# Kernel optimization log

Hardware: AMD Instinct MI355X
Metric: run time of the kernel (lower is better)

The kernel has to match this reference:

```python
import jax, jax.numpy as jnp
import numpy as np

N_NODES = 16384
N_EDGES = 65536
N_GRAPHS = 512
F_XD = 78
HEADS = 10
HID = F_XD * HEADS  # 780
SEQ = 1000
EMB = 100
VOCAB = 8000
NF = 32
KS = 8
CLEN = EMB - KS + 1  # 93
OUT_DIM = 128


def setup_inputs():
    key = jax.random.key(0)
    keys = jax.random.split(key, 32)
    it = iter(keys)

    def rn(shape, scale=0.05):
        return jax.random.normal(next(it), shape, dtype=jnp.float32) * scale

    x = jax.random.normal(next(it), (N_NODES, F_XD), dtype=jnp.float32)
    edge_index = jax.random.randint(next(it), (2, N_EDGES), 0, N_NODES)
    batch = jnp.sort(jax.random.randint(next(it), (N_NODES,), 0, N_GRAPHS))
    target = jax.random.randint(next(it), (N_GRAPHS, SEQ), 0, VOCAB)
    return {
        "x": x, "edge_index": edge_index, "batch": batch, "target": target,
        "gat_w": rn((F_XD, HID)), "gat_att_src": rn((HEADS, F_XD)),
        "gat_att_dst": rn((HEADS, F_XD)), "gat_b": rn((HID,)),
        "gcn_w": rn((HID, HID)), "gcn_b": rn((HID,)),
        "fcg1_w": rn((2 * HID, 1500)), "fcg1_b": rn((1500,)),
        "fcg2_w": rn((1500, OUT_DIM)), "fcg2_b": rn((OUT_DIM,)),
        "emb_w": rn((VOCAB, EMB), 1.0),
        "conv_w": rn((NF, SEQ, KS)), "conv_b": rn((NF,)),
        "fcxt_w": rn((NF * CLEN, OUT_DIM)), "fcxt_b": rn((OUT_DIM,)),
        "mlp1_w": rn((2 * OUT_DIM, 1024)), "mlp1_b": rn((1024,)),
        "mlp2_w": rn((1024, 512)), "mlp2_b": rn((512,)),
        "mlp3_w": rn((512, 1)), "mlp3_b": rn((1,)),
    }


def _forward(edge_index, batch, target, x, gat_w, gat_att_src, gat_att_dst, gat_b,
             gcn_w, gcn_b, fcg1_w, fcg1_b, fcg2_w, fcg2_b, emb_w, conv_w, conv_b,
             fcxt_w, fcxt_b, mlp1_w, mlp1_b, mlp2_w, mlp2_b, mlp3_w, mlp3_b):
    loops = jnp.arange(N_NODES)
    src = jnp.concatenate([edge_index[0], loops])  # add self-loops (PyG default)
    dst = jnp.concatenate([edge_index[1], loops])
    # --- GATConv(78 -> 78, heads=10, concat) ---
    xh = (x @ gat_w).reshape(N_NODES, HEADS, F_XD)
    a_src = jnp.einsum('nhc,hc->nh', xh, gat_att_src)
    a_dst = jnp.einsum('nhc,hc->nh', xh, gat_att_dst)
    e = jax.nn.leaky_relu(a_src[src] + a_dst[dst], 0.2)  # [E+N, H]
    emax = jax.ops.segment_max(e, dst, num_segments=N_NODES)
    ee = jnp.exp(e - emax[dst])
    den = jax.ops.segment_sum(ee, dst, num_segments=N_NODES)
    coef = ee / den[dst]  # segment softmax over incoming edges
    h = jax.ops.segment_sum(xh[src] * coef[:, :, None], dst, num_segments=N_NODES)
    h = jax.nn.relu(h.reshape(N_NODES, HID) + gat_b)
    # --- GCNConv(780 -> 780), symmetric normalization with self-loops ---
    hw = h @ gcn_w
    deg = jax.ops.segment_sum(jnp.ones((src.shape[0],), hw.dtype), dst, num_segments=N_NODES)
    dinv = jax.lax.rsqrt(jnp.maximum(deg, 1.0))  # deg >= 1 due to self-loops
    g = jax.ops.segment_sum(hw[src] * (dinv[src] * dinv[dst])[:, None], dst,
                            num_segments=N_NODES) + gcn_b
    g = jax.nn.relu(g)
    # --- global max / mean pool per graph ---
    gmp = jax.ops.segment_max(g, batch, num_segments=N_GRAPHS)
    cnt = jax.ops.segment_sum(jnp.ones((N_NODES,), g.dtype), batch, num_segments=N_GRAPHS)
    gap = jax.ops.segment_sum(g, batch, num_segments=N_GRAPHS) / jnp.maximum(cnt, 1.0)[:, None]
    d = jnp.concatenate([gmp, gap], axis=1)  # [B, 1560]
    d = jax.nn.relu(d @ fcg1_w + fcg1_b)     # dropout = eval-mode no-op
    d = d @ fcg2_w + fcg2_b                  # [B, 128]
    # --- protein branch: embedding + Conv1d(in=1000, out=32, k=8) + fc ---
    emb = emb_w[target]  # [B, SEQ=1000, EMB=100]
    c = jax.lax.conv_general_dilated(emb, conv_w, (1,), 'VALID',
                                     dimension_numbers=('NCH', 'OIH', 'NCH'))
    c = c + conv_b[None, :, None]            # [B, 32, 93]
    p = c.reshape(N_GRAPHS, NF * CLEN) @ fcxt_w + fcxt_b  # [B, 128]
    # --- fused MLP head: 256 -> 1024 -> 512 -> 1 ---
    o = jnp.concatenate([d, p], axis=1)
    o = jax.nn.relu(o @ mlp1_w + mlp1_b)
    o = jax.nn.relu(o @ mlp2_w + mlp2_b)
    return o @ mlp3_w + mlp3_b               # [B, 1]


def reference(x, edge_index, batch, target, gat_w, gat_att_src, gat_att_dst, gat_b,
              gcn_w, gcn_b, fcg1_w, fcg1_b, fcg2_w, fcg2_b, emb_w, conv_w, conv_b,
              fcxt_w, fcxt_b, mlp1_w, mlp1_b, mlp2_w, mlp2_b, mlp3_w, mlp3_b):
    return _forward(edge_index, batch, target, x, gat_w, gat_att_src, gat_att_dst,
                    gat_b, gcn_w, gcn_b, fcg1_w, fcg1_b, fcg2_w, fcg2_b, emb_w,
                    conv_w, conv_b, fcxt_w, fcxt_b, mlp1_w, mlp1_b, mlp2_w, mlp2_b,
                    mlp3_w, mlp3_b)
```

## Files before the change

### kernel.cpp

```cpp
#include <hip/hip_runtime.h>

#define NN 16384
#define NE 65536
#define NT 81920
#define NG 512
#define NH 10
#define FX 78
#define HD 780
#define SEQ 1000
#define EMB 100
#define NF 32
#define KS 8
#define CLEN 93

typedef __bf16 bf16x8 __attribute__((ext_vector_type(8)));
typedef float  f32x4  __attribute__((ext_vector_type(4)));

__global__ __launch_bounds__(256)
void cast_pad_a(const float* __restrict__ in, __bf16* __restrict__ out,
                int M, int K, int Kp)
{
    size_t idx = (size_t)blockIdx.x*256 + threadIdx.x;
    if (idx >= (size_t)M*Kp) return;
    int r = idx / Kp, c = idx % Kp;
    out[idx] = (c < K) ? (__bf16)in[(size_t)r*K + c] : (__bf16)0.f;
}

__global__ __launch_bounds__(256)
void cast_pad_bt(const float* __restrict__ B, __bf16* __restrict__ out,
                 int K, int N, int Kp, int Np)
{
    size_t idx = (size_t)blockIdx.x*256 + threadIdx.x;
    if (idx >= (size_t)Np*Kp) return;
    int n = idx / Kp, k = idx % Kp;
    out[idx] = (n < N && k < K) ? (__bf16)B[(size_t)k*N + n] : (__bf16)0.f;
}

#define BKP 40
template<bool BIAS, bool RELU, bool BF16OUT>
__global__ __launch_bounds__(256)
void gemm_mfma(const __bf16* __restrict__ A, const __bf16* __restrict__ Bt,
               const float* __restrict__ bias, void* __restrict__ Cv,
               int M, int N, int Kp, int ldc, int Nz)
{
    __shared__ __align__(16) __bf16 As[128*BKP];
    __shared__ __align__(16) __bf16 Bs[128*BKP];
    const int tid = threadIdx.x;
    const int row0 = blockIdx.y*128, col0 = blockIdx.x*128;
    const int lane = tid & 63, wid = tid >> 6;
    const int wm = wid & 1, wn = wid >> 1;
    const int l15 = lane & 15, lk = lane >> 4;

    f32x4 acc[4][4];
#pragma unroll
    for (int i = 0; i < 4; i++)
#pragma unroll
        for (int j = 0; j < 4; j++) acc[i][j] = (f32x4){0.f,0.f,0.f,0.f};

    for (int k0 = 0; k0 < Kp; k0 += 32) {
        __syncthreads();
#pragma unroll
        for (int it = 0; it < 2; ++it) {
            int c = tid + it*256;
            int r = c >> 2, c16 = c & 3;
            uint4 va = *(const uint4*)(A  + (size_t)(row0+r)*Kp + k0 + c16*8);
            *(uint4*)&As[r*BKP + c16*8] = va;
            uint4 vb = *(const uint4*)(Bt + (size_t)(col0+r)*Kp + k0 + c16*8);
            *(uint4*)&Bs[r*BKP + c16*8] = vb;
        }
        __syncthreads();
        bf16x8 af[4], bfr[4];
#pragma unroll
        for (int i = 0; i < 4; i++) {
            af[i]  = *(const bf16x8*)&As[(wm*64 + i*16 + l15)*BKP + lk*8];
            bfr[i] = *(const bf16x8*)&Bs[(wn*64 + i*16 + l15)*BKP + lk*8];
        }
#pragma unroll
        for (int i = 0; i < 4; i++)
#pragma unroll
            for (int j = 0; j < 4; j++)
                acc[i][j] = __builtin_amdgcn_mfma_f32_16x16x32_bf16(af[i], bfr[j], acc[i][j], 0, 0, 0);
    }

#pragma unroll
    for (int i = 0; i < 4; i++) {
        int rbase = row0 + wm*64 + i*16 + lk*4;
#pragma unroll
        for (int j = 0; j < 4; j++) {
            int cc = col0 + wn*64 + j*16 + l15;
            if (cc >= Nz) continue;
            bool real = cc < N;
            float bv = (BIAS && real) ? bias[cc] : 0.f;
#pragma unroll
            for (int r = 0; r < 4; r++) {
                float v = real ? (acc[i][j][r] + bv) : 0.f;
                if (RELU) v = v > 0.f ? v : 0.f;
                if (BF16OUT) ((__bf16*)Cv)[(size_t)(rbase + r)*ldc + cc] = (__bf16)v;
                else         ((float*) Cv)[(size_t)(rbase + r)*ldc + cc] = v;
            }
        }
    }
}

__global__ __launch_bounds__(256)
void gemm_mfma_splitk(const __bf16* __restrict__ A, const __bf16* __restrict__ Bt,
                      float* __restrict__ part, int M, int Kp, int ldp, int ksteps)
{
    __shared__ __align__(16) __bf16 As[128*BKP];
    __shared__ __align__(16) __bf16 Bs[128*BKP];
    const int tid = threadIdx.x;
    const int row0 = blockIdx.y*128, col0 = blockIdx.x*128;
    const int s = blockIdx.z;
    const int lane = tid & 63, wid = tid >> 6;
    const int wm = wid & 1, wn = wid >> 1;
    const int l15 = lane & 15, lk = lane >> 4;

    const int T = Kp >> 5;
    int kb = s*ksteps, ke = kb + ksteps;
    if (ke > T) ke = T;

    f32x4 acc[4][4];
#pragma unroll
    for (int i = 0; i < 4; i++)
#pragma unroll
        for (int j = 0; j < 4; j++) acc[i][j] = (f32x4){0.f,0.f,0.f,0.f};

    for (int kk = kb; kk < ke; kk++) {
        int k0 = kk*32;
        __syncthreads();
#pragma unroll
        for (int it = 0; it < 2; ++it) {
            int c = tid + it*256;
            int r = c >> 2, c16 = c & 3;
            uint4 va = *(const uint4*)(A  + (size_t)(row0+r)*Kp + k0 + c16*8);
            *(uint4*)&As[r*BKP + c16*8] = va;
            uint4 vb = *(const uint4*)(Bt + (size_t)(col0+r)*Kp + k0 + c16*8);
            *(uint4*)&Bs[r*BKP + c16*8] = vb;
        }
        __syncthreads();
        bf16x8 af[4], bfr[4];
#pragma unroll
        for (int i = 0; i < 4; i++) {
            af[i]  = *(const bf16x8*)&As[(wm*64 + i*16 + l15)*BKP + lk*8];
            bfr[i] = *(const bf16x8*)&Bs[(wn*64 + i*16 + l15)*BKP + lk*8];
        }
#pragma unroll
        for (int i = 0; i < 4; i++)
#pragma unroll
            for (int j = 0; j < 4; j++)
                acc[i][j] = __builtin_amdgcn_mfma_f32_16x16x32_bf16(af[i], bfr[j], acc[i][j], 0, 0, 0);
    }

#pragma unroll
    for (int i = 0; i < 4; i++) {
        int rbase = row0 + wm*64 + i*16 + lk*4;
#pragma unroll
        for (int j = 0; j < 4; j++) {
            int cc = col0 + wn*64 + j*16 + l15;
#pragma unroll
            for (int r = 0; r < 4; r++)
                part[((size_t)s*M + rbase + r)*ldp + cc] = acc[i][j][r];
        }
    }
}

template<bool RELU>
__global__ __launch_bounds__(256)
void reduce_splitk(const float* __restrict__ part, const float* __restrict__ bias,
                   __bf16* __restrict__ C, int M, int N, int ldp, int S,
                   int ldc, int Nz)
{
    int idx = blockIdx.x*256 + threadIdx.x;
    int nc4 = Nz >> 2;
    if (idx >= M*nc4) return;
    int r = idx / nc4, c = (idx - r*nc4)*4;
    float4 a = {0.f,0.f,0.f,0.f};
    for (int s = 0; s < S; s++) {
        float4 v = *(const float4*)(part + ((size_t)s*M + r)*ldp + c);
        a.x += v.x; a.y += v.y; a.z += v.z; a.w += v.w;
    }
    float vv[4] = {a.x, a.y, a.z, a.w};
    __bf16 o4[4];
#pragma unroll
    for (int j = 0; j < 4; j++) {
        float v = 0.f;
        if (c + j < N) {
            v = vv[j] + bias[c+j];
            if (RELU) v = v > 0.f ? v : 0.f;
        }
        o4[j] = (__bf16)v;
    }
    *(uint2*)&C[(size_t)r*ldc + c] = *(uint2*)o4;
}

__global__ __launch_bounds__(256)
void attn_logits(const __bf16* __restrict__ xh, const float* __restrict__ att_s,
                 const float* __restrict__ att_d,
                 float* __restrict__ a_src, float* __restrict__ a_dst)
{
    int idx = blockIdx.x*256 + threadIdx.x;
    if (idx >= NN*NH) return;
    int n = idx / NH, h = idx % NH;
    const __bf16* xr = xh + (size_t)n*800 + h*FX;
    const float* as = att_s + h*FX;
    const float* ad = att_d + h*FX;
    float s1 = 0.f, s2 = 0.f;
    for (int c = 0; c < FX; c++) {
        float v = (float)xr[c];
        s1 = fmaf(v, as[c], s1);
        s2 = fmaf(v, ad[c], s2);
    }
    a_src[idx] = s1;
    a_dst[idx] = s2;
}

__global__ void edge_count(const int* __restrict__ ei, int* __restrict__ deg)
{
    int e = blockIdx.x*256 + threadIdx.x;
    if (e >= NT) return;
    int dst = (e < NE) ? ei[NE + e] : (e - NE);
    atomicAdd(&deg[dst], 1);
}

__global__ __launch_bounds__(1024)
void scan_kernel(const int* __restrict__ deg, int* __restrict__ offs, int* __restrict__ cursor)
{
    __shared__ int part[1024];
    int tid = threadIdx.x;
    int base = tid*16;
    int v[16]; int ssum = 0;
#pragma unroll
    for (int j = 0; j < 16; j++) { v[j] = deg[base+j]; ssum += v[j]; }
    part[tid] = ssum;
    __syncthreads();
    for (int d = 1; d < 1024; d <<= 1) {
        int t = (tid >= d) ? part[tid-d] : 0;
        __syncthreads();
        part[tid] += t;
        __syncthreads();
    }
    int run = (tid == 0) ? 0 : part[tid-1];
#pragma unroll
    for (int j = 0; j < 16; j++) { offs[base+j] = run; cursor[base+j] = run; run += v[j]; }
    if (tid == 1023) offs[NN] = run;
}

__global__ void edge_scatter(const int* __restrict__ ei, int* __restrict__ cursor,
                             int* __restrict__ csr)
{
    int e = blockIdx.x*256 + threadIdx.x;
    if (e >= NT) return;
    int src, dst;
    if (e < NE) { src = ei[e]; dst = ei[NE + e]; }
    else        { src = e - NE; dst = e - NE; }
    int pos = atomicAdd(&cursor[dst], 1);
    csr[pos] = src;
}

__global__ void dinv_kernel(const int* __restrict__ offs, float* __restrict__ dinv)
{
    int n = blockIdx.x*256 + threadIdx.x;
    if (n >= NN) return;
    int d = offs[n+1] - offs[n];
    dinv[n] = rsqrtf((float)(d > 0 ? d : 1));
}

__global__ __launch_bounds__(256)
void gat_agg(const __bf16* __restrict__ xh, const float* __restrict__ a_src,
             const float* __restrict__ a_dst, const float* __restrict__ gat_b,
             const int* __restrict__ offs, const int* __restrict__ csr,
             __bf16* __restrict__ hbf)
{
    int n = blockIdx.x*4 + (threadIdx.x >> 6);
    if (n >= NN) return;
    int lane = threadIdx.x & 63;
    bool act = lane < 60;
    int h   = act ? (lane / 6) : 0;
    int sub = act ? (lane % 6) : 0;
    int cbase = h*FX + sub*13;
    int off = offs[n], end = offs[n+1];
    float adn = a_dst[n*NH + h];

    float m = -3.0e38f;
    for (int i = off; i < end; i++) {
        int s = csr[i];
        float ev = a_src[s*NH + h] + adn;
        ev = ev > 0.f ? ev : 0.2f*ev;
        m = fmaxf(m, ev);
    }
    float den = 0.f;
    float acc[13];
#pragma unroll
    for (int j = 0; j < 13; j++) acc[j] = 0.f;
    for (int i = off; i < end; i++) {
        int s = csr[i];
        float ev = a_src[s*NH + h] + adn;
        ev = ev > 0.f ? ev : 0.2f*ev;
        float ee = __expf(ev - m);
        den += ee;
        const __bf16* xr = xh + (size_t)s*800 + cbase;
#pragma unroll
        for (int j = 0; j < 13; j++) acc[j] = fmaf((float)xr[j], ee, acc[j]);
    }
    if (act) {
        float inv = 1.f / den;
        const float* bb = gat_b + cbase;
        __bf16* op = hbf + (size_t)n*800 + cbase;
#pragma unroll
        for (int j = 0; j < 13; j++) {
            float v = fmaf(acc[j], inv, bb[j]);
            op[j] = (__bf16)(v > 0.f ? v : 0.f);
        }
    } else {
        __bf16* op = hbf + (size_t)n*800 + 780 + (lane - 60)*5;
#pragma unroll
        for (int j = 0; j < 5; j++) op[j] = (__bf16)0.f;
    }
}

__global__ __launch_bounds__(256)
void gcn_agg(const __bf16* __restrict__ hw, const float* __restrict__ dinv,
             const float* __restrict__ gcn_b, const int* __restrict__ offs,
             const int* __restrict__ csr, __bf16* __restrict__ g)
{
    int n = blockIdx.x*4 + (threadIdx.x >> 6);
    if (n >= NN) return;
    int lane = threadIdx.x & 63;
    int off = offs[n], end = offs[n+1];
    float dn = dinv[n];
    float acc[13];
#pragma unroll
    for (int j = 0; j < 13; j++) acc[j] = 0.f;
    for (int i = off; i < end; i++) {
        int s = csr[i];
        float w = dinv[s] * dn;
        const __bf16* r = hw + (size_t)s*800;
#pragma unroll
        for (int j = 0; j < 13; j++) {
            int c = lane + 64*j;
            if (c < HD) acc[j] = fmaf((float)r[c], w, acc[j]);
        }
    }
    __bf16* op = g + (size_t)n*HD;
#pragma unroll
    for (int j = 0; j < 13; j++) {
        int c = lane + 64*j;
        if (c < HD) {
            float v = acc[j] + gcn_b[c];
            op[c] = (__bf16)(v > 0.f ? v : 0.f);
        }
    }
}

__global__ void gstart_kernel(const int* __restrict__ batch, int* __restrict__ goffs)
{
    int b = blockIdx.x*256 + threadIdx.x;
    if (b > NG) return;
    if (b == NG) { goffs[NG] = NN; return; }
    int lo = 0, hi = NN;
    while (lo < hi) { int mid = (lo+hi) >> 1; if (batch[mid] < b) lo = mid+1; else hi = mid; }
    goffs[b] = lo;
}

__global__ __launch_bounds__(256)
void pool_kernel(const __bf16* __restrict__ g, const int* __restrict__ goffs,
                 __bf16* __restrict__ d)
{
    int b = blockIdx.x;
    int tid = threadIdx.x;
    int s = goffs[b], e = goffs[b+1];
    float mx[4], sm[4];
#pragma unroll
    for (int j = 0; j < 4; j++) { mx[j] = -3.0e38f; sm[j] = 0.f; }
    for (int n = s; n < e; n++) {
        const __bf16* r = g + (size_t)n*HD;
#pragma unroll
        for (int j = 0; j < 4; j++) {
            int c = tid + 256*j;
            if (c < HD) { float v = (float)r[c]; mx[j] = fmaxf(mx[j], v); sm[j] += v; }
        }
    }
    int cnt = e - s;
    float inv = 1.f / (float)(cnt > 0 ? cnt : 1);
#pragma unroll
    for (int j = 0; j < 4; j++) {
        int c = tid + 256*j;
        if (c < HD) {
            d[(size_t)b*1568 + c]      = (__bf16)mx[j];
            d[(size_t)b*1568 + HD + c] = (__bf16)(sm[j] * inv);
        }
    }
    if (tid < 8) d[(size_t)b*1568 + 1560 + tid] = (__bf16)0.f;
}

__global__ __launch_bounds__(256)
void emb_cast(const float* __restrict__ emb_w, __bf16* __restrict__ embbf)
{
    int idx = blockIdx.x*256 + threadIdx.x;
    if (idx >= 8001*112) return;
    int r = idx / 112, c = idx - (idx/112)*112;
    float v = (r < 8000 && c < EMB) ? emb_w[(size_t)r*EMB + c] : 0.f;
    embbf[idx] = (__bf16)v;
}

__global__ __launch_bounds__(256)
void conv_w_repack(const float* __restrict__ conv_w, __bf16* __restrict__ w2)
{
    int idx = blockIdx.x*256 + threadIdx.x;
    if (idx >= 256*1024) return;
    int op = idx >> 10, i = idx & 1023;
    int o = op & 31, k = op >> 5;
    w2[idx] = (i < SEQ) ? (__bf16)conv_w[((size_t)o*SEQ + i)*KS + k] : (__bf16)0.f;
}

#define CP 104
#define SB (112*40)

__global__ __launch_bounds__(512)
void conv_gemm2(const int* __restrict__ target, const __bf16* __restrict__ embbf,
                const __bf16* __restrict__ w2, const float* __restrict__ conv_b,
                __bf16* __restrict__ cbuf)
{
    __shared__ __align__(16) __bf16 Pl[256*CP];
    __bf16* Bs = Pl;
    int* tg = (int*)&Pl[9088];
    const int b = blockIdx.x;
    const int tid = threadIdx.x;
    const int w = tid >> 6, lane = tid & 63;
    const int l15 = lane & 15, lk = lane >> 4;

    for (int i = tid; i < 1024; i += 512)
        tg[i] = ((i < SEQ) ? target[b*SEQ + i] : 8000) * 112;
    __syncthreads();

    const bool st = tid < 448;
    const int sc = tid >> 2, skq = tid & 3;

    ushort sv[8];
    auto stage_load = [&](int p) {
        if (!st) return;
        int kb = p*32 + skq*8;
        const ushort* eb = (const ushort*)embbf;
#pragma unroll
        for (int r = 0; r < 8; r++)
            sv[r] = eb[tg[kb + r] + sc];
    };
    auto stage_write = [&](int buf) {
        if (!st) return;
        *(uint4*)&Bs[buf*SB + sc*40 + skq*8] = *(uint4*)sv;
    };

    f32x4 acc[7][2];
#pragma unroll
    for (int i = 0; i < 7; i++) {
        acc[i][0] = (f32x4){0.f,0.f,0.f,0.f};
        acc[i][1] = (f32x4){0.f,0.f,0.f,0.f};
    }

    const __bf16* w2w0 = w2 + (size_t)(w*32 + l15)*1024 + lk*8;
    const __bf16* w2w1 = w2w0 + (size_t)16*1024;

    stage_load(0);
    stage_write(0);
    int cur = 0;
    for (int p = 0; p < 32; ++p) {
        __syncthreads();
        if (p+1 < 32) stage_load(p+1);
        bf16x8 bf0 = *(const bf16x8*)(w2w0 + p*32);
        bf16x8 bf1 = *(const bf16x8*)(w2w1 + p*32);
        const __bf16* bsc = Bs + cur*SB + lk*8;
        __builtin_amdgcn_s_setprio(1);
#pragma unroll
        for (int mt = 0; mt < 7; mt++) {
            bf16x8 af = *(const bf16x8*)(bsc + (mt*16 + l15)*40);
            acc[mt][0] = __builtin_amdgcn_mfma_f32_16x16x32_bf16(af, bf0, acc[mt][0], 0, 0, 0);
            acc[mt][1] = __builtin_amdgcn_mfma_f32_16x16x32_bf16(af, bf1, acc[mt][1], 0, 0, 0);
        }
        __builtin_amdgcn_s_setprio(0);
        if (p+1 < 32) stage_write(cur^1);
        cur ^= 1;
    }

    __syncthreads();
#pragma unroll
    for (int mt = 0; mt < 7; mt++) {
#pragma unroll
        for (int nt = 0; nt < 2; nt++) {
            int op = w*32 + nt*16 + l15;
            int c0 = mt*16 + lk*4;
            if (c0 >= 100) continue;
            __bf16 o4[4];
#pragma unroll
            for (int rr = 0; rr < 4; rr++) o4[rr] = (__bf16)acc[mt][nt][rr];
            *(uint2*)&Pl[op*CP + c0] = *(uint2*)o4;
        }
    }
    __syncthreads();

    {
        int o = tid & 31, tg16 = tid >> 5;
        float cb = conv_b[o];
#pragma unroll
        for (int j = 0; j < 6; j++) {
            int t = tg16*6 + j;
            if (t >= CLEN) continue;
            float s = cb;
#pragma unroll
            for (int k = 0; k < 8; k++)
                s += (float)Pl[(k*32 + o)*CP + t + k];
            cbuf[(size_t)b*2976 + o*CLEN + t] = (__bf16)s;
        }
    }
}

__global__ __launch_bounds__(256)
void mlp3_dot(const __bf16* __restrict__ o2, const float* __restrict__ w,
              const float* __restrict__ bias, float* __restrict__ out)
{
    int row = blockIdx.x*4 + (threadIdx.x >> 6);
    int lane = threadIdx.x & 63;
    bf16x8 v = *(const bf16x8*)(o2 + (size_t)row*512 + lane*8);
    float4 w0 = *(const float4*)(w + lane*8);
    float4 w1 = *(const float4*)(w + lane*8 + 4);
    float s = (float)v[0]*w0.x + (float)v[1]*w0.y + (float)v[2]*w0.z + (float)v[3]*w0.w
            + (float)v[4]*w1.x + (float)v[5]*w1.y + (float)v[6]*w1.z + (float)v[7]*w1.w;
#pragma unroll
    for (int off = 32; off > 0; off >>= 1) s += __shfl_down(s, off);
    if (lane == 0) out[row] = s + bias[0];
}

extern "C" void kernel_launch(void* const* d_in, const int* in_sizes, int n_in,
                              void* d_out, int out_size, void* d_ws, size_t ws_size,
                              hipStream_t stream)
{
    const float* x      = (const float*)d_in[0];
    const int*   ei     = (const int*)  d_in[1];
    const int*   batch  = (const int*)  d_in[2];
    const int*   target = (const int*)  d_in[3];
    const float* gat_w  = (const float*)d_in[4];
    const float* att_s  = (const float*)d_in[5];
    const float* att_d  = (const float*)d_in[6];
    const float* gat_b  = (const float*)d_in[7];
    const float* gcn_w  = (const float*)d_in[8];
    const float* gcn_b  = (const float*)d_in[9];
    const float* fcg1_w = (const float*)d_in[10];
    const float* fcg1_b = (const float*)d_in[11];
    const float* fcg2_w = (const float*)d_in[12];
    const float* fcg2_b = (const float*)d_in[13];
    const float* emb_w  = (const float*)d_in[14];
    const float* conv_w = (const float*)d_in[15];
    const float* conv_b = (const float*)d_in[16];
    const float* fcxt_w = (const float*)d_in[17];
    const float* fcxt_b = (const float*)d_in[18];
    const float* mlp1_w = (const float*)d_in[19];
    const float* mlp1_b = (const float*)d_in[20];
    const float* mlp2_w = (const float*)d_in[21];
    const float* mlp2_b = (const float*)d_in[22];
    const float* mlp3_w = (const float*)d_in[23];
    const float* mlp3_b = (const float*)d_in[24];
    float* out = (float*)d_out;

    char* ws = (char*)d_ws;
    size_t off = 0;
    auto alloc = [&](size_t bytes) -> char* {
        char* p = ws + off;
        off = (off + bytes + 255) & ~(size_t)255;
        return p;
    };
    __bf16* xhbf  = (__bf16*)alloc((size_t)NN*800*2);
    __bf16* g     = (__bf16*)alloc((size_t)NN*HD*2);
    char*  hbf_rg = alloc((size_t)NN*800*2);
    __bf16* Abf   = (__bf16*)hbf_rg;
    __bf16* hbf   = (__bf16*)hbf_rg;
    float* partial= (float*)hbf_rg;
    __bf16* Btbf  = (__bf16*)alloc((size_t)896*800*2);
    __bf16* wg1   = (__bf16*)alloc((size_t)1536*1568*2);
    __bf16* wg2   = (__bf16*)alloc((size_t)128*1504*2);
    __bf16* wxt   = (__bf16*)alloc((size_t)128*2976*2);
    __bf16* wm1   = (__bf16*)alloc((size_t)1024*256*2);
    __bf16* wm2   = (__bf16*)alloc((size_t)512*1024*2);
    __bf16* convw2= (__bf16*)alloc((size_t)256*1024*2);
    __bf16* embbf = (__bf16*)alloc((size_t)8001*112*2);
    float* a_src  = (float*)alloc((size_t)NN*NH*4);
    float* a_dst  = (float*)alloc((size_t)NN*NH*4);
    int*   deg    = (int*)alloc((size_t)NN*4);
    int*   offs   = (int*)alloc((size_t)(NN+1)*4);
    int*   cursor = (int*)alloc((size_t)NN*4);
    int*   csr    = (int*)alloc((size_t)NT*4);
    float* dinv   = (float*)alloc((size_t)NN*4);
    int*   goffs  = (int*)alloc((size_t)(NG+1)*4);
    __bf16* dpool = (__bf16*)alloc((size_t)NG*1568*2);
    __bf16* d1bf  = (__bf16*)alloc((size_t)NG*1504*2);
    __bf16* cbuf  = (__bf16*)alloc((size_t)NG*NF*CLEN*2);
    __bf16* obuf  = (__bf16*)alloc((size_t)NG*256*2);
    __bf16* o1bf  = (__bf16*)alloc((size_t)NG*1024*2);
    __bf16* o2bf  = (__bf16*)alloc((size_t)NG*512*2);

    __bf16* hwbf = xhbf;

    hipMemsetAsync(deg, 0, (size_t)NN*4, stream);

    emb_cast     <<<dim3((8001*112+255)/256), 256, 0, stream>>>(emb_w, embbf);
    conv_w_repack<<<dim3(1024), 256, 0, stream>>>(conv_w, convw2);
    cast_pad_bt<<<dim3((1536*1568)/256), 256, 0, stream>>>(fcg1_w, wg1, 1560, 1500, 1568, 1536);
    cast_pad_bt<<<dim3((128*1504)/256), 256, 0, stream>>>(fcg2_w, wg2, 1500, 128, 1504, 128);
    cast_pad_bt<<<dim3((128*2976)/256), 256, 0, stream>>>(fcxt_w, wxt, NF*CLEN, 128, 2976, 128);
    cast_pad_bt<<<dim3((1024*256)/256), 256, 0, stream>>>(mlp1_w, wm1, 256, 1024, 256, 1024);
    cast_pad_bt<<<dim3((512*1024)/256), 256, 0, stream>>>(mlp2_w, wm2, 1024, 512, 1024, 512);

    conv_gemm2<<<dim3(NG), 512, 0, stream>>>(target, embbf, convw2, conv_b, cbuf);

    cast_pad_a <<<dim3((NN*96)/256), 256, 0, stream>>>(x, Abf, NN, FX, 96);
    cast_pad_bt<<<dim3((896*96)/256), 256, 0, stream>>>(gat_w, Btbf, FX, HD, 96, 896);
    gemm_mfma<false,false,true>
        <<<dim3(7, NN/128), 256, 0, stream>>>(Abf, Btbf, nullptr, xhbf, NN, HD, 96, 800, 800);
    attn_logits<<<dim3((NN*NH+255)/256), 256, 0, stream>>>(xhbf, att_s, att_d, a_src, a_dst);

    edge_count  <<<dim3(NT/256), 256, 0, stream>>>(ei, deg);
    scan_kernel <<<1, 1024, 0, stream>>>(deg, offs, cursor);
    edge_scatter<<<dim3(NT/256), 256, 0, stream>>>(ei, cursor, csr);
    dinv_kernel <<<dim3(NN/256), 256, 0, stream>>>(offs, dinv);

    gat_agg<<<dim3(NN/4), 256, 0, stream>>>(xhbf, a_src, a_dst, gat_b, offs, csr, hbf);

    cast_pad_bt<<<dim3((896*800)/256), 256, 0, stream>>>(gcn_w, Btbf, HD, HD, 800, 896);
    gemm_mfma<false,false,true>
        <<<dim3(7, NN/128), 256, 0, stream>>>(hbf, Btbf, nullptr, hwbf, NN, HD, 800, 800, 800);
    gcn_agg<<<dim3(NN/4), 256, 0, stream>>>(hwbf, dinv, gcn_b, offs, csr, g);

    gstart_kernel<<<3, 256, 0, stream>>>(batch, goffs);
    pool_kernel<<<NG, 256, 0, stream>>>(g, goffs, dpool);

    gemm_mfma_splitk<<<dim3(12, 4, 4), 256, 0, stream>>>(dpool, wg1, partial, NG, 1568, 1536, 13);
    reduce_splitk<true><<<dim3((NG*(1504/4)+255)/256), 256, 0, stream>>>(partial, fcg1_b, d1bf, NG, 1500, 1536, 4, 1504, 1504);
    gemm_mfma_splitk<<<dim3(1, 4, 12), 256, 0, stream>>>(d1bf, wg2, partial, NG, 1504, 128, 4);
    reduce_splitk<false><<<dim3((NG*32+255)/256), 256, 0, stream>>>(partial, fcg2_b, obuf, NG, 128, 128, 12, 256, 128);
    gemm_mfma_splitk<<<dim3(1, 4, 24), 256, 0, stream>>>(cbuf, wxt, partial, NG, 2976, 128, 4);
    reduce_splitk<false><<<dim3((NG*32+255)/256), 256, 0, stream>>>(partial, fcxt_b, obuf + 128, NG, 128, 128, 24, 256, 128);
    gemm_mfma_splitk<<<dim3(8, 4, 2), 256, 0, stream>>>(obuf, wm1, partial, NG, 256, 1024, 4);
    reduce_splitk<true><<<dim3((NG*256+255)/256), 256, 0, stream>>>(partial, mlp1_b, o1bf, NG, 1024, 1024, 2, 1024, 1024);
    gemm_mfma_splitk<<<dim3(4, 4, 8), 256, 0, stream>>>(o1bf, wm2, partial, NG, 1024, 512, 4);
    reduce_splitk<true><<<dim3((NG*128+255)/256), 256, 0, stream>>>(partial, mlp2_b, o2bf, NG, 512, 512, 8, 512, 512);

    mlp3_dot<<<dim3(NG/4), 256, 0, stream>>>(o2bf, mlp3_w, mlp3_b, out);
}
```

Measured before the change: 417.2 us.

## Merge weight casts into one preprocessing kernel and vectorize conv embedding staging

Replaces the separate cast/pad, embedding cast, conv weight repack and graph-start launches with a single flat-indexed preprocessing kernel. It gives the GAT and GCN weights separate buffers so both can be prepared up front, and folds the dinv computation into the scan kernel. The conv_gemm2 staging now does one 16-byte vector load per embedding row and scatters it into shared memory transposed, where before it did eight scalar gathers. The aim is fewer kernel launches and fewer scalar memory transactions, at the cost of a large branchy kernel and strided shared-memory writes that may bank-conflict.

Measured after the change: 382.1 us. -8.4%, faster.

```diff
diff --git a/kernel.cpp b/kernel.cpp
--- a/kernel.cpp
+++ b/kernel.cpp
@@ -16,25 +16,70 @@
 typedef __bf16 bf16x8 __attribute__((ext_vector_type(8)));
 typedef float  f32x4  __attribute__((ext_vector_type(4)));
 
-__global__ __launch_bounds__(256)
-void cast_pad_a(const float* __restrict__ in, __bf16* __restrict__ out,
-                int M, int K, int Kp)
-{
-    size_t idx = (size_t)blockIdx.x*256 + threadIdx.x;
-    if (idx >= (size_t)M*Kp) return;
-    int r = idx / Kp, c = idx % Kp;
-    out[idx] = (c < K) ? (__bf16)in[(size_t)r*K + c] : (__bf16)0.f;
-}
-
-__global__ __launch_bounds__(256)
-void cast_pad_bt(const float* __restrict__ B, __bf16* __restrict__ out,
-                 int K, int N, int Kp, int Np)
-{
-    size_t idx = (size_t)blockIdx.x*256 + threadIdx.x;
-    if (idx >= (size_t)Np*Kp) return;
-    int n = idx / Kp, k = idx % Kp;
+__device__ inline void bt_one(const float* __restrict__ B, __bf16* __restrict__ out,
+                              long idx, int K, int N, int Kp)
+{
+    int n = idx / Kp, k = idx - (long)(idx / Kp)*Kp;
     out[idx] = (n < N && k < K) ? (__bf16)B[(size_t)k*N + n] : (__bf16)0.f;
 }
+
+__global__ __launch_bounds__(256)
+void preproc_all(const float* __restrict__ emb_w, __bf16* __restrict__ embbf,
+                 const float* __restrict__ conv_w, __bf16* __restrict__ w2,
+                 const float* __restrict__ fcg1_w, __bf16* __restrict__ wg1,
+                 const float* __restrict__ fcg2_w, __bf16* __restrict__ wg2,
+                 const float* __restrict__ fcxt_w, __bf16* __restrict__ wxt,
+                 const float* __restrict__ mlp1_w, __bf16* __restrict__ wm1,
+                 const float* __restrict__ mlp2_w, __bf16* __restrict__ wm2,
+                 const float* __restrict__ x, __bf16* __restrict__ Abf,
+                 const float* __restrict__ gat_w, __bf16* __restrict__ wgat,
+                 const float* __restrict__ gcn_w, __bf16* __restrict__ wgcn,
+                 const int* __restrict__ batch, int* __restrict__ goffs)
+{
+    long idx = (long)blockIdx.x*256 + threadIdx.x;
+    if (idx < 896112L) {
+        int r = idx / 112, c = idx - (long)(idx/112)*112;
+        embbf[idx] = (__bf16)((r < 8000 && c < EMB) ? emb_w[(size_t)r*EMB + c] : 0.f);
+        return;
+    }
+    idx -= 896112L;
+    if (idx < 262144L) {
+        int op = idx >> 10, i = idx & 1023;
+        int o = op & 31, k = op >> 5;
+        w2[idx] = (i < SEQ) ? (__bf16)conv_w[((size_t)o*SEQ + i)*KS + k] : (__bf16)0.f;
+        return;
+    }
+    idx -= 262144L;
+    if (idx < 2408448L) { bt_one(fcg1_w, wg1, idx, 1560, 1500, 1568); return; }
+    idx -= 2408448L;
+    if (idx < 192512L)  { bt_one(fcg2_w, wg2, idx, 1500, 128, 1504); return; }
+    idx -= 192512L;
+    if (idx < 380928L)  { bt_one(fcxt_w, wxt, idx, 2976, 128, 2976); return; }
+    idx -= 380928L;
+    if (idx < 262144L)  { bt_one(mlp1_w, wm1, idx, 256, 1024, 256); return; }
+    idx -= 262144L;
+    if (idx < 524288L)  { bt_one(mlp2_w, wm2, idx, 1024, 512, 1024); return; }
+    idx -= 524288L;
+    if (idx < 1572864L) {
+        int r = idx / 96, c = idx - (long)(idx/96)*96;
+        Abf[idx] = (c < FX) ? (__bf16)x[(size_t)r*FX + c] : (__bf16)0.f;
+        return;
+    }
+    idx -= 1572864L;
+    if (idx < 86016L)   { bt_one(gat_w, wgat, idx, 78, 780, 96); return; }
+    idx -= 86016L;
+    if (idx < 716800L)  { bt_one(gcn_w, wgcn, idx, 780, 780, 800); return; }
+    idx -= 716800L;
+    if (idx <= NG) {
+        int b = (int)idx;
+        if (b == NG) { goffs[NG] = NN; return; }
+        int lo = 0, hi = NN;
+        while (lo < hi) { int mid = (lo+hi) >> 1; if (batch[mid] < b) lo = mid+1; else hi = mid; }
+        goffs[b] = lo;
+    }
+}
+#define PRE_TOTAL 7302256L
+#define PRE_BLOCKS ((PRE_TOTAL + 513 + 255) / 256)
 
 #define BKP 40
 template<bool BIAS, bool RELU, bool BF16OUT>
@@ -223,14 +268,19 @@
 }
 
 __global__ __launch_bounds__(1024)
-void scan_kernel(const int* __restrict__ deg, int* __restrict__ offs, int* __restrict__ cursor)
+void scan_kernel(const int* __restrict__ deg, int* __restrict__ offs,
+                 int* __restrict__ cursor, float* __restrict__ dinv)
 {
     __shared__ int part[1024];
     int tid = threadIdx.x;
     int base = tid*16;
     int v[16]; int ssum = 0;
 #pragma unroll
-    for (int j = 0; j < 16; j++) { v[j] = deg[base+j]; ssum += v[j]; }
+    for (int j = 0; j < 16; j++) {
+        v[j] = deg[base+j];
+        dinv[base+j] = rsqrtf((float)(v[j] > 0 ? v[j] : 1));
+        ssum += v[j];
+    }
     part[tid] = ssum;
     __syncthreads();
     for (int d = 1; d < 1024; d <<= 1) {
@@ -255,14 +305,6 @@
     else        { src = e - NE; dst = e - NE; }
     int pos = atomicAdd(&cursor[dst], 1);
     csr[pos] = src;
-}
-
-__global__ void dinv_kernel(const int* __restrict__ offs, float* __restrict__ dinv)
-{
-    int n = blockIdx.x*256 + threadIdx.x;
-    if (n >= NN) return;
-    int d = offs[n+1] - offs[n];
-    dinv[n] = rsqrtf((float)(d > 0 ? d : 1));
 }
 
 __global__ __launch_bounds__(256)
@@ -352,16 +394,6 @@
     }
 }
 
-__global__ void gstart_kernel(const int* __restrict__ batch, int* __restrict__ goffs)
-{
-    int b = blockIdx.x*256 + threadIdx.x;
-    if (b > NG) return;
-    if (b == NG) { goffs[NG] = NN; return; }
-    int lo = 0, hi = NN;
-    while (lo < hi) { int mid = (lo+hi) >> 1; if (batch[mid] < b) lo = mid+1; else hi = mid; }
-    goffs[b] = lo;
-}
-
 __global__ __launch_bounds__(256)
 void pool_kernel(const __bf16* __restrict__ g, const int* __restrict__ goffs,
                  __bf16* __restrict__ d)
@@ -393,26 +425,6 @@
     if (tid < 8) d[(size_t)b*1568 + 1560 + tid] = (__bf16)0.f;
 }
 
-__global__ __launch_bounds__(256)
-void emb_cast(const float* __restrict__ emb_w, __bf16* __restrict__ embbf)
-{
-    int idx = blockIdx.x*256 + threadIdx.x;
-    if (idx >= 8001*112) return;
-    int r = idx / 112, c = idx - (idx/112)*112;
-    float v = (r < 8000 && c < EMB) ? emb_w[(size_t)r*EMB + c] : 0.f;
-    embbf[idx] = (__bf16)v;
-}
-
-__global__ __launch_bounds__(256)
-void conv_w_repack(const float* __restrict__ conv_w, __bf16* __restrict__ w2)
-{
-    int idx = blockIdx.x*256 + threadIdx.x;
-    if (idx >= 256*1024) return;
-    int op = idx >> 10, i = idx & 1023;
-    int o = op & 31, k = op >> 5;
-    w2[idx] = (i < SEQ) ? (__bf16)conv_w[((size_t)o*SEQ + i)*KS + k] : (__bf16)0.f;
-}
-
 #define CP 104
 #define SB (112*40)
 
@@ -423,7 +435,7 @@
 {
     __shared__ __align__(16) __bf16 Pl[256*CP];
     __bf16* Bs = Pl;
-    int* tg = (int*)&Pl[9088];
+    int* tg = (int*)&Pl[2*SB];
     const int b = blockIdx.x;
     const int tid = threadIdx.x;
     const int w = tid >> 6, lane = tid & 63;
@@ -434,20 +446,20 @@
     __syncthreads();
 
     const bool st = tid < 448;
-    const int sc = tid >> 2, skq = tid & 3;
-
-    ushort sv[8];
+    const int sr  = tid & 31;
+    const int sch = tid >> 5;
+
+    uint4 sv;
     auto stage_load = [&](int p) {
         if (!st) return;
-        int kb = p*32 + skq*8;
-        const ushort* eb = (const ushort*)embbf;
-#pragma unroll
-        for (int r = 0; r < 8; r++)
-            sv[r] = eb[tg[kb + r] + sc];
+        sv = *(const uint4*)((const ushort*)embbf + tg[p*32 + sr] + sch*8);
     };
     auto stage_write = [&](int buf) {
         if (!st) return;
-        *(uint4*)&Bs[buf*SB + sc*40 + skq*8] = *(uint4*)sv;
+        const __bf16* s8 = (const __bf16*)&sv;
+        __bf16* base = &Bs[buf*SB + (sch*8)*40 + sr];
+#pragma unroll
+        for (int j = 0; j < 8; j++) base[j*40] = s8[j];
     };
 
     f32x4 acc[7][2];
@@ -573,7 +585,8 @@
     __bf16* Abf   = (__bf16*)hbf_rg;
     __bf16* hbf   = (__bf16*)hbf_rg;
     float* partial= (float*)hbf_rg;
-    __bf16* Btbf  = (__bf16*)alloc((size_t)896*800*2);
+    __bf16* wgat  = (__bf16*)alloc((size_t)896*96*2);
+    __bf16* wgcn  = (__bf16*)alloc((size_t)896*800*2);
     __bf16* wg1   = (__bf16*)alloc((size_t)1536*1568*2);
     __bf16* wg2   = (__bf16*)alloc((size_t)128*1504*2);
     __bf16* wxt   = (__bf16*)alloc((size_t)128*2976*2);
@@ -600,35 +613,26 @@
 
     hipMemsetAsync(deg, 0, (size_t)NN*4, stream);
 
-    emb_cast     <<<dim3((8001*112+255)/256), 256, 0, stream>>>(emb_w, embbf);
-    conv_w_repack<<<dim3(1024), 256, 0, stream>>>(conv_w, convw2);
-    cast_pad_bt<<<dim3((1536*1568)/256), 256, 0, stream>>>(fcg1_w, wg1, 1560, 1500, 1568, 1536);
-    cast_pad_bt<<<dim3((128*1504)/256), 256, 0, stream>>>(fcg2_w, wg2, 1500, 128, 1504, 128);
-    cast_pad_bt<<<dim3((128*2976)/256), 256, 0, stream>>>(fcxt_w, wxt, NF*CLEN, 128, 2976, 128);
-    cast_pad_bt<<<dim3((1024*256)/256), 256, 0, stream>>>(mlp1_w, wm1, 256, 1024, 256, 1024);
-    cast_pad_bt<<<dim3((512*1024)/256), 256, 0, stream>>>(mlp2_w, wm2, 1024, 512, 1024, 512);
+    preproc_all<<<dim3((unsigned)PRE_BLOCKS), 256, 0, stream>>>(
+        emb_w, embbf, conv_w, convw2, fcg1_w, wg1, fcg2_w, wg2, fcxt_w, wxt,
+        mlp1_w, wm1, mlp2_w, wm2, x, Abf, gat_w, wgat, gcn_w, wgcn, batch, goffs);
 
     conv_gemm2<<<dim3(NG), 512, 0, stream>>>(target, embbf, convw2, conv_b, cbuf);
 
-    cast_pad_a <<<dim3((NN*96)/256), 256, 0, stream>>>(x, Abf, NN, FX, 96);
-    cast_pad_bt<<<dim3((896*96)/256), 256, 0, stream>>>(gat_w, Btbf, FX, HD, 96, 896);
     gemm_mfma<false,false,true>
-        <<<dim3(7, NN/128), 256, 0, stream>>>(Abf, Btbf, nullptr, xhbf, NN, HD, 96, 800, 800);
+        <<<dim3(7, NN/128), 256, 0, stream>>>(Abf, wgat, nullptr, xhbf, NN, HD, 96, 800, 800);
     attn_logits<<<dim3((NN*NH+255)/256), 256, 0, stream>>>(xhbf, att_s, att_d, a_src, a_dst);
 
     edge_count  <<<dim3(NT/256), 256, 0, stream>>>(ei, deg);
-    scan_kernel <<<1, 1024, 0, stream>>>(deg, offs, cursor);
+    scan_kernel <<<1, 1024, 0, stream>>>(deg, offs, cursor, dinv);
     edge_scatter<<<dim3(NT/256), 256, 0, stream>>>(ei, cursor, csr);
-    dinv_kernel <<<dim3(NN/256), 256, 0, stream>>>(offs, dinv);
 
     gat_agg<<<dim3(NN/4), 256, 0, stream>>>(xhbf, a_src, a_dst, gat_b, offs, csr, hbf);
 
-    cast_pad_bt<<<dim3((896*800)/256), 256, 0, stream>>>(gcn_w, Btbf, HD, HD, 800, 896);
     gemm_mfma<false,false,true>
-        <<<dim3(7, NN/128), 256, 0, stream>>>(hbf, Btbf, nullptr, hwbf, NN, HD, 800, 800, 800);
+        <<<dim3(7, NN/128), 256, 0, stream>>>(hbf, wgcn, nullptr, hwbf, NN, HD, 800, 800, 800);
     gcn_agg<<<dim3(NN/4), 256, 0, stream>>>(hwbf, dinv, gcn_b, offs, csr, g);
 
-    gstart_kernel<<<3, 256, 0, stream>>>(batch, goffs);
     pool_kernel<<<NG, 256, 0, stream>>>(g, goffs, dpool);
 
     gemm_mfma_splitk<<<dim3(12, 4, 4), 256, 0, stream>>>(dpool, wg1, partial, NG, 1568, 1536, 13);
```
